# Kernel tuning notes

Measured on AMD Instinct MI355X. Metric: run time of the kernel, lower is better.

Reference implementation:

```python
import jax, jax.numpy as jnp
import numpy as np

B, S, D, DFF = 4, 2048, 1024, 4096
EPS = 1e-5


def layernorm(x, g, b):
    mu = jnp.mean(x, axis=-1, keepdims=True)
    var = jnp.mean(jnp.square(x - mu), axis=-1, keepdims=True)
    return (x - mu) * jax.lax.rsqrt(var + EPS) * g + b


def setup_inputs() -> dict:
    key = jax.random.key(0)
    ks = jax.random.split(key, 4)
    hidden_state = jax.random.normal(ks[0], (B, S, D), dtype=jnp.float32)
    attention_mask = jnp.zeros((B, 1, S), dtype=jnp.float32)  # additive mask
    w1 = jax.random.normal(ks[1], (D, DFF), dtype=jnp.float32) * (1.0 / np.sqrt(D))
    b1 = jnp.zeros((DFF,), dtype=jnp.float32)
    w2 = jax.random.normal(ks[2], (DFF, D), dtype=jnp.float32) * (1.0 / np.sqrt(DFF))
    b2 = jnp.zeros((D,), dtype=jnp.float32)
    ln1_g = jnp.ones((D,), dtype=jnp.float32)
    ln1_b = jnp.zeros((D,), dtype=jnp.float32)
    ln2_g = jnp.ones((D,), dtype=jnp.float32)
    ln2_b = jnp.zeros((D,), dtype=jnp.float32)
    return dict(hidden_state=hidden_state, attention_mask=attention_mask,
                w1=w1, b1=b1, w2=w2, b2=b2,
                ln1_g=ln1_g, ln1_b=ln1_b, ln2_g=ln2_g, ln2_b=ln2_b)


def reference(hidden_state, attention_mask, w1, b1, w2, b2, ln1_g, ln1_b, ln2_g, ln2_b):
    x = hidden_state
    d = jnp.asarray(x.shape[-1], x.dtype)
    # hand-rolled single-head attention: q=k=v=x (source forward ignores QKV projections)
    scores = jnp.einsum('bqd,bkd->bqk', x, x) / jnp.sqrt(d) + attention_mask  # [B,S,S]
    attn = jax.nn.softmax(scores, axis=-1)
    attn_out = jnp.einsum('bqk,bkd->bqd', attn, x)
    h = layernorm(x + attn_out, ln1_g, ln1_b)
    # FFN: dense -> exact GELU -> linear_2
    ffn = jnp.einsum('bsf,fd->bsd', jax.nn.gelu(jnp.einsum('bsd,df->bsf', h, w1) + b1, approximate=False), w2) + b2
    return layernorm(h + ffn, ln2_g, ln2_b)
```

## Files before the change

### kernel.cpp

```cpp
#include <hip/hip_runtime.h>
#include <hip/hip_bf16.h>
#include <math.h>

#define LN_EPS 1e-5f

typedef short short8 __attribute__((ext_vector_type(8)));
typedef float floatx4 __attribute__((ext_vector_type(4)));

__device__ inline unsigned short f2bf(float f) {
    unsigned int u = __float_as_uint(f);
    u += 0x7fff + ((u >> 16) & 1);
    return (unsigned short)(u >> 16);
}

__device__ inline void gl_lds16(const unsigned short* g, unsigned short* l) {
    __builtin_amdgcn_global_load_lds(
        (__attribute__((address_space(1))) const void*)g,
        (__attribute__((address_space(3))) void*)l, 16, 0, 0);
}

__device__ inline float gelu_f(float v) {
    float u2 = 2.0f * v * (0.7978845608f + 0.0356774081f * v * v);
    float t  = 1.0f - 2.0f / (__expf(u2) + 1.0f);
    return 0.5f * v * (1.0f + t);
}

#define CFENCE asm volatile("" ::: "memory")

template<int EPI, int BN>
__global__ __launch_bounds__(512, 2) void gemm8p(
    const unsigned short* __restrict__ A, const unsigned short* __restrict__ B,
    const float* __restrict__ bias, const float* __restrict__ resid,
    void* __restrict__ Cptr,
    int M, int N, int K, long sA, long sB, long sC, long sBias, float scale)
{
    static_assert(BN == 256 || BN == 128, "BN must be 256 or 128");
    constexpr int WC = BN / 4;
    constexpr int NT = WC / 16;
    constexpr int NH = NT / 2;

    __shared__ alignas(16) unsigned short lds_a[2][2][256 * 32];
    __shared__ alignas(16) unsigned short lds_b[2][2][BN * 32];

    const int tid  = threadIdx.x;
    const int lane = tid & 63;
    const int wave = tid >> 6;
    const int quad = lane >> 4;
    const int l16  = lane & 15;
    const int wm = wave >> 2;
    const int wn = wave & 3;

    const int nwg = gridDim.x * gridDim.y * gridDim.z;
    int lin = blockIdx.x + gridDim.x * (blockIdx.y + gridDim.y * blockIdx.z);
    if ((nwg & 7) == 0) lin = (lin & 7) * (nwg >> 3) + (lin >> 3);
    const int bx = lin % gridDim.x;
    const int byz = lin / gridDim.x;
    const int by = byz % gridDim.y;
    const int bz = byz / gridDim.y;

    const int tile_m = by * 256;
    const int tile_n = bx * BN;
    const int batch  = bz;

    const unsigned short* Ab = A + (size_t)batch * sA;
    const unsigned short* Bb = B + (size_t)batch * sB;

    const int srow = tid >> 2;
    const int scs  = ((tid & 3) ^ ((tid & 32) ? 2 : 0)) * 8;
    const unsigned short* gA = Ab + (size_t)(tile_m + srow) * K + scs;
    const unsigned short* gB = Bb + (size_t)(tile_n + srow) * K + scs;
    const int ldst = tid * 8;

    const int kcs   = (quad * 8) ^ ((l16 & 8) << 1);
    const int abase = (wm * 128 + l16) * 32 + kcs;
    const int bbase = (wn * WC  + l16) * 32 + kcs;

    floatx4 acc[8][NT];
    const floatx4 zero = {0.f, 0.f, 0.f, 0.f};
#pragma unroll
    for (int i = 0; i < 8; i++)
#pragma unroll
        for (int j = 0; j < NT; j++) acc[i][j] = zero;

    auto stageA = [&](int buf, int h, int k0) {
        const unsigned short* s = gA + (size_t)h * 128 * K + k0;
        gl_lds16(s,      &lds_a[buf][0][h * 4096 + ldst]);
        gl_lds16(s + 32, &lds_a[buf][1][h * 4096 + ldst]);
    };
    auto stageB = [&](int buf, int h, int k0) {
        const unsigned short* s = gB + (size_t)h * 128 * K + k0;
        gl_lds16(s,      &lds_b[buf][0][h * 4096 + ldst]);
        gl_lds16(s + 32, &lds_b[buf][1][h * 4096 + ldst]);
    };

    const int nt = K >> 6;

    stageA(0, 0, 0); stageA(0, 1, 0);
    stageB(0, 0, 0);
    if constexpr (BN == 256) stageB(0, 1, 0);
    if (nt > 1) {
        stageB(1, 0, 64);
        if constexpr (BN == 256) stageB(1, 1, 64);
        if constexpr (BN == 256) { asm volatile("s_waitcnt vmcnt(4)" ::: "memory"); }
        else                     { asm volatile("s_waitcnt vmcnt(2)" ::: "memory"); }
    } else {
        asm volatile("s_waitcnt vmcnt(0)" ::: "memory");
    }
    __builtin_amdgcn_s_barrier(); CFENCE;

    int cur = 0;

    if constexpr (BN == 128) {
        for (int t = 0; t < nt; ++t) {
            const int k0 = t * 64;
            short8 afr[4][2], bfr[2][2];

#pragma unroll
            for (int i = 0; i < 4; i++)
#pragma unroll
                for (int kh = 0; kh < 2; kh++)
                    afr[i][kh] = *(const short8*)&lds_a[cur][kh][abase + i * 512];
#pragma unroll
            for (int j = 0; j < 2; j++)
#pragma unroll
                for (int kh = 0; kh < 2; kh++)
                    bfr[j][kh] = *(const short8*)&lds_b[cur][kh][bbase + j * 512];
            if (t + 1 < nt) { stageA(cur ^ 1, 0, k0 + 64); stageA(cur ^ 1, 1, k0 + 64); }
            CFENCE; __builtin_amdgcn_s_barrier(); CFENCE;
            __builtin_amdgcn_s_setprio(1);
#pragma unroll
            for (int i = 0; i < 4; i++)
#pragma unroll
                for (int j = 0; j < 2; j++)
#pragma unroll
                    for (int kh = 0; kh < 2; kh++)
                        acc[i][j] = __builtin_amdgcn_mfma_f32_16x16x32_bf16(
                            bfr[j][kh], afr[i][kh], acc[i][j], 0, 0, 0);
            __builtin_amdgcn_s_setprio(0);
            CFENCE; __builtin_amdgcn_s_barrier(); CFENCE;

#pragma unroll
            for (int i = 0; i < 4; i++)
#pragma unroll
                for (int kh = 0; kh < 2; kh++)
                    afr[i][kh] = *(const short8*)&lds_a[cur][kh][abase + (4 + i) * 512];
            if (t + 2 < nt) stageB(cur, 0, k0 + 128);
            __builtin_amdgcn_s_setprio(1);
#pragma unroll
            for (int i = 0; i < 4; i++)
#pragma unroll
                for (int j = 0; j < 2; j++)
#pragma unroll
                    for (int kh = 0; kh < 2; kh++)
                        acc[4 + i][j] = __builtin_amdgcn_mfma_f32_16x16x32_bf16(
                            bfr[j][kh], afr[i][kh], acc[4 + i][j], 0, 0, 0);
            __builtin_amdgcn_s_setprio(0);
            if (t + 3 <= nt) {
                asm volatile("s_waitcnt vmcnt(2)" ::: "memory");
                __builtin_amdgcn_s_barrier(); CFENCE;
            } else if (t + 2 == nt) {
                asm volatile("s_waitcnt vmcnt(0)" ::: "memory");
                __builtin_amdgcn_s_barrier(); CFENCE;
            }
            cur ^= 1;
        }
    } else {
        for (int t = 0; t < nt; ++t) {
            const int k0 = t * 64;
            short8 afr[4][2], bfrA[NH][2], bfrB[NH][2];

#pragma unroll
            for (int i = 0; i < 4; i++)
#pragma unroll
                for (int kh = 0; kh < 2; kh++)
                    afr[i][kh] = *(const short8*)&lds_a[cur][kh][abase + i * 512];
#pragma unroll
            for (int j = 0; j < NH; j++)
#pragma unroll
                for (int kh = 0; kh < 2; kh++)
                    bfrA[j][kh] = *(const short8*)&lds_b[cur][kh][bbase + j * 512];
            if (t + 1 < nt) stageA(cur ^ 1, 0, k0 + 64);
            CFENCE; __builtin_amdgcn_s_barrier(); CFENCE;
            __builtin_amdgcn_s_setprio(1);
#pragma unroll
            for (int i = 0; i < 4; i++)
#pragma unroll
                for (int j = 0; j < NH; j++)
#pragma unroll
                    for (int kh = 0; kh < 2; kh++)
                        acc[i][j] = __builtin_amdgcn_mfma_f32_16x16x32_bf16(
                            bfrA[j][kh], afr[i][kh], acc[i][j], 0, 0, 0);
            __builtin_amdgcn_s_setprio(0);
            CFENCE; __builtin_amdgcn_s_barrier(); CFENCE;

#pragma unroll
            for (int j = 0; j < NH; j++)
#pragma unroll
                for (int kh = 0; kh < 2; kh++)
                    bfrB[j][kh] = *(const short8*)&lds_b[cur][kh][bbase + (NH + j) * 512];
            if (t + 1 < nt) stageA(cur ^ 1, 1, k0 + 64);
            CFENCE; __builtin_amdgcn_s_barrier(); CFENCE;
            __builtin_amdgcn_s_setprio(1);
#pragma unroll
            for (int i = 0; i < 4; i++)
#pragma unroll
                for (int j = 0; j < NH; j++)
#pragma unroll
                    for (int kh = 0; kh < 2; kh++)
                        acc[i][NH + j] = __builtin_amdgcn_mfma_f32_16x16x32_bf16(
                            bfrB[j][kh], afr[i][kh], acc[i][NH + j], 0, 0, 0);
            __builtin_amdgcn_s_setprio(0);
            CFENCE; __builtin_amdgcn_s_barrier(); CFENCE;

#pragma unroll
            for (int i = 0; i < 4; i++)
#pragma unroll
                for (int kh = 0; kh < 2; kh++)
                    afr[i][kh] = *(const short8*)&lds_a[cur][kh][abase + (4 + i) * 512];
            if (t + 2 < nt) stageB(cur, 0, k0 + 128);
            CFENCE; __builtin_amdgcn_s_barrier(); CFENCE;
            __builtin_amdgcn_s_setprio(1);
#pragma unroll
            for (int i = 0; i < 4; i++)
#pragma unroll
                for (int j = 0; j < NH; j++)
#pragma unroll
                    for (int kh = 0; kh < 2; kh++)
                        acc[4 + i][NH + j] = __builtin_amdgcn_mfma_f32_16x16x32_bf16(
                            bfrB[j][kh], afr[i][kh], acc[4 + i][NH + j], 0, 0, 0);
            __builtin_amdgcn_s_setprio(0);
            CFENCE; __builtin_amdgcn_s_barrier(); CFENCE;

            if (t + 2 < nt) stageB(cur, 1, k0 + 128);
            __builtin_amdgcn_s_setprio(1);
#pragma unroll
            for (int i = 0; i < 4; i++)
#pragma unroll
                for (int j = 0; j < NH; j++)
#pragma unroll
                    for (int kh = 0; kh < 2; kh++)
                        acc[4 + i][j] = __builtin_amdgcn_mfma_f32_16x16x32_bf16(
                            bfrA[j][kh], afr[i][kh], acc[4 + i][j], 0, 0, 0);
            __builtin_amdgcn_s_setprio(0);
            if (t + 3 <= nt) {
                asm volatile("s_waitcnt vmcnt(4)" ::: "memory");
                __builtin_amdgcn_s_barrier(); CFENCE;
            } else if (t + 2 == nt) {
                asm volatile("s_waitcnt vmcnt(0)" ::: "memory");
                __builtin_amdgcn_s_barrier(); CFENCE;
            }
            cur ^= 1;
        }
    }

#pragma unroll
    for (int i = 0; i < 8; i++) {
        const int row = tile_m + wm * 128 + i * 16 + l16;
#pragma unroll
        for (int j = 0; j < NT; j++) {
            const int colb = tile_n + wn * WC + j * 16 + quad * 4;
            float v[4];
#pragma unroll
            for (int r = 0; r < 4; r++) v[r] = acc[i][j][r];

            if (EPI == 3) {
                float4 mv = *(const float4*)&bias[(size_t)batch * sBias + colb];
                v[0] = v[0] * scale + mv.x;  v[1] = v[1] * scale + mv.y;
                v[2] = v[2] * scale + mv.z;  v[3] = v[3] * scale + mv.w;
            }
            if (EPI == 2 || EPI == 5) {
                float4 bv = *(const float4*)&bias[colb];
                v[0] += bv.x; v[1] += bv.y; v[2] += bv.z; v[3] += bv.w;
            }
            if (EPI == 2) {
#pragma unroll
                for (int r = 0; r < 4; r++) v[r] = gelu_f(v[r]);
            }
            if (EPI == 4 || EPI == 5) {
                float4 rv = *(const float4*)&resid[(size_t)batch * sC +
                                                   (size_t)row * N + colb];
                v[0] += rv.x; v[1] += rv.y; v[2] += rv.z; v[3] += rv.w;
            }

            if (EPI == 2 || EPI == 3) {
                unsigned short* C = (unsigned short*)Cptr + (size_t)batch * sC;
                ushort4 h4;
                h4.x = f2bf(v[0]); h4.y = f2bf(v[1]);
                h4.z = f2bf(v[2]); h4.w = f2bf(v[3]);
                *(ushort4*)(C + (size_t)row * N + colb) = h4;
            } else {
                float* C = (float*)Cptr + (size_t)batch * sC;
                float4 f4 = {v[0], v[1], v[2], v[3]};
                *(float4*)(C + (size_t)row * N + colb) = f4;
            }
        }
    }
}

__global__ __launch_bounds__(256) void x_prep_kernel(
    const float* __restrict__ in, unsigned short* __restrict__ straight,
    unsigned short* __restrict__ transposed, int R, int C, long sIn)
{
    __shared__ float tile[32][33];
    const int tc = blockIdx.x * 32, tr = blockIdx.y * 32;
    const float* src = in + (size_t)blockIdx.z * sIn;
    unsigned short* dstS = straight   + (size_t)blockIdx.z * sIn;
    unsigned short* dstT = transposed + (size_t)blockIdx.z * sIn;
    const int tx = threadIdx.x & 31, ty = threadIdx.x >> 5;
#pragma unroll
    for (int i = 0; i < 4; i++) {
        float val = src[(size_t)(tr + ty + i * 8) * C + tc + tx];
        tile[ty + i * 8][tx] = val;
        dstS[(size_t)(tr + ty + i * 8) * C + tc + tx] = f2bf(val);
    }
    __syncthreads();
#pragma unroll
    for (int i = 0; i < 4; i++)
        dstT[(size_t)(tc + ty + i * 8) * R + tr + tx] = f2bf(tile[tx][ty + i * 8]);
}

__global__ __launch_bounds__(256) void transpose_cvt_kernel(
    const float* __restrict__ in, unsigned short* __restrict__ out, int R, int C)
{
    __shared__ float tile[32][33];
    const int tc = blockIdx.x * 32, tr = blockIdx.y * 32;
    const int tx = threadIdx.x & 31, ty = threadIdx.x >> 5;
#pragma unroll
    for (int i = 0; i < 4; i++)
        tile[ty + i * 8][tx] = in[(size_t)(tr + ty + i * 8) * C + tc + tx];
    __syncthreads();
#pragma unroll
    for (int i = 0; i < 4; i++)
        out[(size_t)(tc + ty + i * 8) * R + tr + tx] = f2bf(tile[tx][ty + i * 8]);
}

__global__ __launch_bounds__(256) void softmax_bf16_kernel(
    const unsigned short* __restrict__ scores, unsigned short* __restrict__ probs,
    int S)
{
    __shared__ float red[4];
    const int row = blockIdx.x;
    const unsigned short* p = scores + (size_t)row * S;
    unsigned short* pr      = probs  + (size_t)row * S;
    const int tid  = threadIdx.x;
    const int lane = tid & 63;
    const int wav  = tid >> 6;

    uint4 raw = *(const uint4*)(p + tid * 8);
    float v[8];
    v[0] = __uint_as_float(raw.x << 16); v[1] = __uint_as_float(raw.x & 0xffff0000u);
    v[2] = __uint_as_float(raw.y << 16); v[3] = __uint_as_float(raw.y & 0xffff0000u);
    v[4] = __uint_as_float(raw.z << 16); v[5] = __uint_as_float(raw.z & 0xffff0000u);
    v[6] = __uint_as_float(raw.w << 16); v[7] = __uint_as_float(raw.w & 0xffff0000u);

    float mx = v[0];
#pragma unroll
    for (int k = 1; k < 8; k++) mx = fmaxf(mx, v[k]);
#pragma unroll
    for (int off = 32; off > 0; off >>= 1) mx = fmaxf(mx, __shfl_down(mx, off));
    if (lane == 0) red[wav] = mx;
    __syncthreads();
    mx = fmaxf(fmaxf(red[0], red[1]), fmaxf(red[2], red[3]));
    __syncthreads();

    float s = 0.f;
#pragma unroll
    for (int k = 0; k < 8; k++) { v[k] = __expf(v[k] - mx); s += v[k]; }
#pragma unroll
    for (int off = 32; off > 0; off >>= 1) s += __shfl_down(s, off);
    if (lane == 0) red[wav] = s;
    __syncthreads();
    s = red[0] + red[1] + red[2] + red[3];
    float inv = 1.0f / s;

    uint4 o;
    o.x = (unsigned)f2bf(v[0] * inv) | ((unsigned)f2bf(v[1] * inv) << 16);
    o.y = (unsigned)f2bf(v[2] * inv) | ((unsigned)f2bf(v[3] * inv) << 16);
    o.z = (unsigned)f2bf(v[4] * inv) | ((unsigned)f2bf(v[5] * inv) << 16);
    o.w = (unsigned)f2bf(v[6] * inv) | ((unsigned)f2bf(v[7] * inv) << 16);
    *(uint4*)(pr + tid * 8) = o;
}

template<int WRITE_BF16>
__global__ __launch_bounds__(256) void ln_kernel(
    const float* __restrict__ X,
    const float* __restrict__ g, const float* __restrict__ bta,
    float* __restrict__ out, unsigned short* __restrict__ out16, int D)
{
    __shared__ float red[8];
    const int row = blockIdx.x;
    const float* x = X + (size_t)row * D;
    const int tid  = threadIdx.x;
    const int lane = tid & 63;
    const int wav  = tid >> 6;

    float4 a = *(const float4*)(x + tid * 4);
    float v0 = a.x, v1 = a.y, v2 = a.z, v3 = a.w;

    float s1 = v0 + v1 + v2 + v3;
    float s2 = v0 * v0 + v1 * v1 + v2 * v2 + v3 * v3;
#pragma unroll
    for (int off = 32; off > 0; off >>= 1) {
        s1 += __shfl_down(s1, off);
        s2 += __shfl_down(s2, off);
    }
    if (lane == 0) { red[wav] = s1; red[4 + wav] = s2; }
    __syncthreads();
    s1 = red[0] + red[1] + red[2] + red[3];
    s2 = red[4] + red[5] + red[6] + red[7];
    const float mu  = s1 / (float)D;
    const float var = s2 / (float)D - mu * mu;
    const float rs  = rsqrtf(var + LN_EPS);

    float4 gg = *(const float4*)(g + tid * 4);
    float4 bb = *(const float4*)(bta + tid * 4);
    float4 r;
    r.x = (v0 - mu) * rs * gg.x + bb.x;
    r.y = (v1 - mu) * rs * gg.y + bb.y;
    r.z = (v2 - mu) * rs * gg.z + bb.z;
    r.w = (v3 - mu) * rs * gg.w + bb.w;
    *(float4*)(out + (size_t)row * D + tid * 4) = r;
    if (WRITE_BF16) {
        ushort4 h;
        h.x = f2bf(r.x); h.y = f2bf(r.y); h.z = f2bf(r.z); h.w = f2bf(r.w);
        *(ushort4*)(out16 + (size_t)row * D + tid * 4) = h;
    }
}

extern "C" void kernel_launch(void* const* d_in, const int* in_sizes, int n_in,
                              void* d_out, int out_size, void* d_ws, size_t ws_size,
                              hipStream_t stream) {
    (void)in_sizes; (void)n_in; (void)out_size; (void)ws_size;
    const float* x    = (const float*)d_in[0];
    const float* mask = (const float*)d_in[1];
    const float* w1   = (const float*)d_in[2];
    const float* b1   = (const float*)d_in[3];
    const float* w2   = (const float*)d_in[4];
    const float* b2   = (const float*)d_in[5];
    const float* ln1g = (const float*)d_in[6];
    const float* ln1b = (const float*)d_in[7];
    const float* ln2g = (const float*)d_in[8];
    const float* ln2b = (const float*)d_in[9];
    float* out = (float*)d_out;

    const int B = 4, S = 2048, D = 1024, DFF = 4096;
    const size_t MB = 1024 * 1024;

    char* ws = (char*)d_ws;
    unsigned short* scoresb = (unsigned short*)ws;
    unsigned short* act     = (unsigned short*)ws;
    unsigned short* xb      = (unsigned short*)(ws + 32 * MB);
    unsigned short* probs   = (unsigned short*)(ws + 32 * MB);
    float*          hbuf    = (float*)(ws + 64 * MB);
    unsigned short* hb16    = (unsigned short*)(ws + 96 * MB);
    unsigned short* w1T     = (unsigned short*)(ws + 112 * MB);
    unsigned short* w2T     = (unsigned short*)(ws + 120 * MB);
    unsigned short* xTb     = (unsigned short*)d_out;
    float*          fsum    = (float*)d_out;

    x_prep_kernel<<<dim3(D / 32, S / 32, B), 256, 0, stream>>>(
        x, xb, xTb, S, D, (long)S * D);
    transpose_cvt_kernel<<<dim3(DFF / 32, D / 32, 1), 256, 0, stream>>>(w1, w1T, D, DFF);
    transpose_cvt_kernel<<<dim3(D / 32, DFF / 32, 1), 256, 0, stream>>>(w2, w2T, DFF, D);

    hipLaunchKernelGGL((gemm8p<3, 256>), dim3(S / 256, S / 256, B), dim3(512), 0, stream,
                       xb, xb, mask, (const float*)nullptr, (void*)scoresb,
                       S, S, D, (long)S * D, (long)S * D, (long)S * S, (long)S, 0.03125f);
    softmax_bf16_kernel<<<B * S, 256, 0, stream>>>(scoresb, probs, S);
    hipLaunchKernelGGL((gemm8p<4, 128>), dim3(D / 128, S / 256, B), dim3(512), 0, stream,
                       probs, xTb, (const float*)nullptr, x, (void*)hbuf,
                       S, D, S, (long)S * S, (long)D * S, (long)S * D, 0L, 0.f);
    hipLaunchKernelGGL((ln_kernel<1>), dim3(B * S), dim3(256), 0, stream,
                       hbuf, ln1g, ln1b, hbuf, hb16, D);
    hipLaunchKernelGGL((gemm8p<2, 256>), dim3(DFF / 256, (B * S) / 256, 1), dim3(512), 0, stream,
                       hb16, w1T, b1, (const float*)nullptr, (void*)act,
                       B * S, DFF, D, 0L, 0L, 0L, 0L, 0.f);
    hipLaunchKernelGGL((gemm8p<5, 128>), dim3(D / 128, (B * S) / 256, 1), dim3(512), 0, stream,
                       act, w2T, b2, hbuf, (void*)fsum,
                       B * S, D, DFF, 0L, 0L, 0L, 0L, 0.f);
    hipLaunchKernelGGL((ln_kernel<0>), dim3(B * S), dim3(256), 0, stream,
                       fsum, ln2g, ln2b, out, (unsigned short*)nullptr, D);
}
```

Before: 409.9 us.

## Prefetch A half-tile two iterations ahead in the BN=256 GEMM pipeline

Restructures the BN=256 main loop's global-to-LDS prefetch schedule. The first A half of the next-next tile is now issued together with the second B half in the last phase, and the second A half of the next tile is issued in the first phase. The prologue and the vmcnt waits (now 6) are adjusted to match the deeper queue of outstanding loads. The MFMA loops are also reordered to put kh outermost, so consecutive instructions avoid back-to-back dependence on the same accumulator. The aim is to hide more global load latency behind MFMA work, at the cost of more in-flight loads and more fragile wait-count bookkeeping.

```diff
diff --git a/kernel.cpp b/kernel.cpp
--- a/kernel.cpp
+++ b/kernel.cpp
@@ -37,7 +37,6 @@
     static_assert(BN == 256 || BN == 128, "BN must be 256 or 128");
     constexpr int WC = BN / 4;
     constexpr int NT = WC / 16;
-    constexpr int NH = NT / 2;
 
     __shared__ alignas(16) unsigned short lds_a[2][2][256 * 32];
     __shared__ alignas(16) unsigned short lds_b[2][2][BN * 32];
@@ -94,23 +93,19 @@
     };
 
     const int nt = K >> 6;
-
-    stageA(0, 0, 0); stageA(0, 1, 0);
-    stageB(0, 0, 0);
-    if constexpr (BN == 256) stageB(0, 1, 0);
-    if (nt > 1) {
-        stageB(1, 0, 64);
-        if constexpr (BN == 256) stageB(1, 1, 64);
-        if constexpr (BN == 256) { asm volatile("s_waitcnt vmcnt(4)" ::: "memory"); }
-        else                     { asm volatile("s_waitcnt vmcnt(2)" ::: "memory"); }
-    } else {
-        asm volatile("s_waitcnt vmcnt(0)" ::: "memory");
-    }
-    __builtin_amdgcn_s_barrier(); CFENCE;
-
     int cur = 0;
 
     if constexpr (BN == 128) {
+        stageA(0, 0, 0); stageA(0, 1, 0);
+        stageB(0, 0, 0);
+        if (nt > 1) {
+            stageB(1, 0, 64);
+            asm volatile("s_waitcnt vmcnt(2)" ::: "memory");
+        } else {
+            asm volatile("s_waitcnt vmcnt(0)" ::: "memory");
+        }
+        __builtin_amdgcn_s_barrier(); CFENCE;
+
         for (int t = 0; t < nt; ++t) {
             const int k0 = t * 64;
             short8 afr[4][2], bfr[2][2];
@@ -165,9 +160,20 @@
             cur ^= 1;
         }
     } else {
+        stageA(0, 0, 0); stageA(0, 1, 0);
+        stageB(0, 0, 0); stageB(0, 1, 0);
+        if (nt > 1) {
+            stageB(1, 0, 64); stageB(1, 1, 64);
+            stageA(1, 0, 64);
+            asm volatile("s_waitcnt vmcnt(6)" ::: "memory");
+        } else {
+            asm volatile("s_waitcnt vmcnt(0)" ::: "memory");
+        }
+        __builtin_amdgcn_s_barrier(); CFENCE;
+
         for (int t = 0; t < nt; ++t) {
             const int k0 = t * 64;
-            short8 afr[4][2], bfrA[NH][2], bfrB[NH][2];
+            short8 afr[4][2], bfrA[2][2], bfrB[2][2];
 
 #pragma unroll
             for (int i = 0; i < 4; i++)
@@ -175,40 +181,39 @@
                 for (int kh = 0; kh < 2; kh++)
                     afr[i][kh] = *(const short8*)&lds_a[cur][kh][abase + i * 512];
 #pragma unroll
-            for (int j = 0; j < NH; j++)
+            for (int j = 0; j < 2; j++)
 #pragma unroll
                 for (int kh = 0; kh < 2; kh++)
                     bfrA[j][kh] = *(const short8*)&lds_b[cur][kh][bbase + j * 512];
-            if (t + 1 < nt) stageA(cur ^ 1, 0, k0 + 64);
-            CFENCE; __builtin_amdgcn_s_barrier(); CFENCE;
-            __builtin_amdgcn_s_setprio(1);
-#pragma unroll
-            for (int i = 0; i < 4; i++)
-#pragma unroll
-                for (int j = 0; j < NH; j++)
-#pragma unroll
-                    for (int kh = 0; kh < 2; kh++)
+            if (t + 1 < nt) stageA(cur ^ 1, 1, k0 + 64);
+            CFENCE; __builtin_amdgcn_s_barrier(); CFENCE;
+            __builtin_amdgcn_s_setprio(1);
+#pragma unroll
+            for (int kh = 0; kh < 2; kh++)
+#pragma unroll
+                for (int i = 0; i < 4; i++)
+#pragma unroll
+                    for (int j = 0; j < 2; j++)
                         acc[i][j] = __builtin_amdgcn_mfma_f32_16x16x32_bf16(
                             bfrA[j][kh], afr[i][kh], acc[i][j], 0, 0, 0);
             __builtin_amdgcn_s_setprio(0);
             CFENCE; __builtin_amdgcn_s_barrier(); CFENCE;
 
 #pragma unroll
-            for (int j = 0; j < NH; j++)
-#pragma unroll
-                for (int kh = 0; kh < 2; kh++)
-                    bfrB[j][kh] = *(const short8*)&lds_b[cur][kh][bbase + (NH + j) * 512];
-            if (t + 1 < nt) stageA(cur ^ 1, 1, k0 + 64);
-            CFENCE; __builtin_amdgcn_s_barrier(); CFENCE;
-            __builtin_amdgcn_s_setprio(1);
-#pragma unroll
-            for (int i = 0; i < 4; i++)
-#pragma unroll
-                for (int j = 0; j < NH; j++)
-#pragma unroll
-                    for (int kh = 0; kh < 2; kh++)
-                        acc[i][NH + j] = __builtin_amdgcn_mfma_f32_16x16x32_bf16(
-                            bfrB[j][kh], afr[i][kh], acc[i][NH + j], 0, 0, 0);
+            for (int j = 0; j < 2; j++)
+#pragma unroll
+                for (int kh = 0; kh < 2; kh++)
+                    bfrB[j][kh] = *(const short8*)&lds_b[cur][kh][bbase + (2 + j) * 512];
+            CFENCE; __builtin_amdgcn_s_barrier(); CFENCE;
+            __builtin_amdgcn_s_setprio(1);
+#pragma unroll
+            for (int kh = 0; kh < 2; kh++)
+#pragma unroll
+                for (int i = 0; i < 4; i++)
+#pragma unroll
+                    for (int j = 0; j < 2; j++)
+                        acc[i][2 + j] = __builtin_amdgcn_mfma_f32_16x16x32_bf16(
+                            bfrB[j][kh], afr[i][kh], acc[i][2 + j], 0, 0, 0);
             __builtin_amdgcn_s_setprio(0);
             CFENCE; __builtin_amdgcn_s_barrier(); CFENCE;
 
@@ -221,29 +226,29 @@
             CFENCE; __builtin_amdgcn_s_barrier(); CFENCE;
             __builtin_amdgcn_s_setprio(1);
 #pragma unroll
-            for (int i = 0; i < 4; i++)
-#pragma unroll
-                for (int j = 0; j < NH; j++)
-#pragma unroll
-                    for (int kh = 0; kh < 2; kh++)
-                        acc[4 + i][NH + j] = __builtin_amdgcn_mfma_f32_16x16x32_bf16(
-                            bfrB[j][kh], afr[i][kh], acc[4 + i][NH + j], 0, 0, 0);
-            __builtin_amdgcn_s_setprio(0);
-            CFENCE; __builtin_amdgcn_s_barrier(); CFENCE;
-
-            if (t + 2 < nt) stageB(cur, 1, k0 + 128);
-            __builtin_amdgcn_s_setprio(1);
-#pragma unroll
-            for (int i = 0; i < 4; i++)
-#pragma unroll
-                for (int j = 0; j < NH; j++)
-#pragma unroll
-                    for (int kh = 0; kh < 2; kh++)
+            for (int kh = 0; kh < 2; kh++)
+#pragma unroll
+                for (int i = 0; i < 4; i++)
+#pragma unroll
+                    for (int j = 0; j < 2; j++)
+                        acc[4 + i][2 + j] = __builtin_amdgcn_mfma_f32_16x16x32_bf16(
+                            bfrB[j][kh], afr[i][kh], acc[4 + i][2 + j], 0, 0, 0);
+            __builtin_amdgcn_s_setprio(0);
+            CFENCE; __builtin_amdgcn_s_barrier(); CFENCE;
+
+            if (t + 2 < nt) { stageB(cur, 1, k0 + 128); stageA(cur, 0, k0 + 128); }
+            __builtin_amdgcn_s_setprio(1);
+#pragma unroll
+            for (int kh = 0; kh < 2; kh++)
+#pragma unroll
+                for (int i = 0; i < 4; i++)
+#pragma unroll
+                    for (int j = 0; j < 2; j++)
                         acc[4 + i][j] = __builtin_amdgcn_mfma_f32_16x16x32_bf16(
                             bfrA[j][kh], afr[i][kh], acc[4 + i][j], 0, 0, 0);
             __builtin_amdgcn_s_setprio(0);
             if (t + 3 <= nt) {
-                asm volatile("s_waitcnt vmcnt(4)" ::: "memory");
+                asm volatile("s_waitcnt vmcnt(6)" ::: "memory");
                 __builtin_amdgcn_s_barrier(); CFENCE;
             } else if (t + 2 == nt) {
                 asm volatile("s_waitcnt vmcnt(0)" ::: "memory");
```

Measured after the change: 417.0 us. Within noise of the previous version (+1.7%).
